# Kernel tuning notes

Measured on AMD Instinct MI355X. Metric: run time of the kernel, lower is better.

Reference implementation:

```python
import jax, jax.numpy as jnp
import numpy as np

B, P, C, O = 16, 19248, 81, 32
POS_THRESH, NEG_THRESH, NEGPOS_RATIO = 0.5, 0.4, 3
BBOX_ALPHA, CONF_ALPHA = 1.5, 1.0
VAR0, VAR1 = 0.1, 0.2  # SSD encoding variances


def setup_inputs() -> dict:
    key = jax.random.key(0)
    ks = jax.random.split(key, 7)
    loc_data = jax.random.normal(ks[0], (B, P, 4), dtype=jnp.float32)
    conf_data = jax.random.normal(ks[1], (B, P, C), dtype=jnp.float32)
    # priors in center form (cx, cy, w, h), all positive
    cxcy = jax.random.uniform(ks[2], (P, 2), minval=0.05, maxval=0.95)
    wh = jax.random.uniform(ks[3], (P, 2), minval=0.05, maxval=0.30)
    priors = jnp.concatenate([cxcy, wh], axis=-1).astype(jnp.float32)
    # gt boxes in point form (x1, y1, x2, y2), valid and inside [0,1]
    gcxcy = jax.random.uniform(ks[4], (B, O, 2), minval=0.1, maxval=0.9)
    gwh = jax.random.uniform(ks[5], (B, O, 2), minval=0.05, maxval=0.4)
    gt_boxes = jnp.clip(jnp.concatenate([gcxcy - gwh / 2, gcxcy + gwh / 2], axis=-1), 0.0, 1.0).astype(jnp.float32)
    gt_labels = jax.random.randint(ks[6], (B, O), 0, C - 1, dtype=jnp.int32)  # 0..79, bg is class 0 after +1
    return {"loc_data": loc_data, "conf_data": conf_data, "priors": priors,
            "gt_boxes": gt_boxes, "gt_labels": gt_labels}


def _point_form(boxes):
    # center form (cx,cy,w,h) -> point form (x1,y1,x2,y2)
    return jnp.concatenate([boxes[:, :2] - boxes[:, 2:] / 2,
                            boxes[:, :2] + boxes[:, 2:] / 2], axis=-1)


def _jaccard(a, b):
    # a: [O,4] point form, b: [P,4] point form -> IoU [O,P]
    lt = jnp.maximum(a[:, None, :2], b[None, :, :2])
    rb = jnp.minimum(a[:, None, 2:], b[None, :, 2:])
    inter = jnp.prod(jnp.clip(rb - lt, 0.0, None), axis=-1)
    area_a = jnp.prod(a[:, 2:] - a[:, :2], axis=-1)[:, None]
    area_b = jnp.prod(b[:, 2:] - b[:, :2], axis=-1)[None, :]
    return inter / (area_a + area_b - inter)


def _encode(matched, priors):
    # matched: [P,4] point form gt; priors: [P,4] center form
    g_cxcy = ((matched[:, :2] + matched[:, 2:]) / 2 - priors[:, :2]) / (VAR0 * priors[:, 2:])
    g_wh = jnp.log((matched[:, 2:] - matched[:, :2]) / priors[:, 2:]) / VAR1
    return jnp.concatenate([g_cxcy, g_wh], axis=-1)


def _match_one(truths, labels, priors):
    # truths: [O,4] point form, labels: [O] int, priors: [P,4] center form
    overlaps = _jaccard(truths, _point_form(priors))          # [O,P]
    best_truth_overlap = overlaps.max(axis=0)                  # [P]
    best_truth_idx = overlaps.argmax(axis=0)                   # [P]
    best_prior_idx = overlaps.argmax(axis=1)                   # [O]
    # ensure every gt is matched to its best prior
    best_truth_overlap = best_truth_overlap.at[best_prior_idx].set(2.0)
    best_truth_idx = best_truth_idx.at[best_prior_idx].set(jnp.arange(truths.shape[0]))
    matched = truths[best_truth_idx]                           # [P,4]
    conf = labels[best_truth_idx] + 1                          # [P]
    conf = jnp.where(best_truth_overlap < POS_THRESH, -1, conf)  # neutral
    conf = jnp.where(best_truth_overlap < NEG_THRESH, 0, conf)   # background
    loc = _encode(matched, priors)                             # [P,4]
    return loc, conf


def _multibox_loss(loc_data, conf_data, priors, gt_boxes, gt_labels):
    loc_t, conf_t = jax.vmap(_match_one, in_axes=(0, 0, None))(gt_boxes, gt_labels, priors)
    pos = conf_t > 0                                           # [B,P]
    # --- localization: smooth L1 on positives ---
    d = jnp.abs(loc_data - loc_t)
    sl1 = jnp.where(d < 1.0, 0.5 * d * d, d - 0.5)
    loss_B = jnp.sum(sl1 * pos[..., None].astype(sl1.dtype)) * BBOX_ALPHA
    # --- OHEM confidence loss ---
    logZ = jax.nn.logsumexp(conf_data, axis=-1)                # [B,P]
    loss_c = logZ - conf_data[..., 0]                          # log_sum_exp - background logit
    loss_c = jnp.where(pos | (conf_t < 0), 0.0, loss_c)
    order = jnp.argsort(-loss_c, axis=1)                       # descending
    idx_rank = jnp.argsort(order, axis=1)                      # rank of each prior
    num_pos = jnp.sum(pos, axis=1, keepdims=True)              # [B,1]
    num_neg = jnp.clip(NEGPOS_RATIO * num_pos, None, P - 1)
    neg = (idx_rank < num_neg) & (~pos) & (conf_t >= 0)
    ce = logZ - jnp.take_along_axis(conf_data, jnp.maximum(conf_t, 0)[..., None], axis=-1)[..., 0]
    loss_C = jnp.sum(ce * (pos | neg).astype(ce.dtype)) * CONF_ALPHA
    total_num_pos = jnp.sum(pos).astype(loc_data.dtype)
    return jnp.stack([loss_B, loss_C]) / total_num_pos


def reference(loc_data, conf_data, priors, gt_boxes, gt_labels):
    return _multibox_loss(loc_data, conf_data, priors, gt_boxes, gt_labels)
```

## Files before the change

kernel.cpp:

```cpp
#include <hip/hip_runtime.h>
#include <math.h>

#define B_ 16
#define P_ 19248
#define C_ 81
#define O_ 32
#define POS_TH 0.5f
#define NEG_TH 0.4f
#define RPB 128
#define TPB 1024
#define PQ  4812
#define BP_BLK (B_ * O_ * 4)
#define BT_BPB 76
#define OT 1024
#define NJ 19

__device__ __forceinline__ float sl1(float x) {
    float d = fabsf(x);
    return (d < 1.0f) ? 0.5f * d * d : d - 0.5f;
}

__device__ __forceinline__ float iou_gt_prior(float4 t, float4 pr) {
    float px1 = pr.x - pr.z * 0.5f;
    float py1 = pr.y - pr.w * 0.5f;
    float px2 = pr.x + pr.z * 0.5f;
    float py2 = pr.y + pr.w * 0.5f;
    float ltx = fmaxf(t.x, px1), lty = fmaxf(t.y, py1);
    float rbx = fminf(t.z, px2), rby = fminf(t.w, py2);
    float iw = fmaxf(rbx - ltx, 0.0f), ih = fmaxf(rby - lty, 0.0f);
    float inter = iw * ih;
    float area_t = (t.z - t.x) * (t.w - t.y);
    float area_p = (px2 - px1) * (py2 - py1);
    return inter / (area_t + area_p - inter);
}

template <int PER>
__device__ __forceinline__ void pick_top(const int* __restrict__ h, int kk, int tid,
                                         int* s_bin, int* s_kk, int* wsum) {
    const int lane = tid & 63, wid = tid >> 6;
    const int base = tid * PER;
    int v[PER]; int s = 0;
    #pragma unroll
    for (int j = 0; j < PER; ++j) { v[j] = h[base + j]; s += v[j]; }
    int x = s;
    #pragma unroll
    for (int d = 1; d < 64; d <<= 1) {
        int y = __shfl_down(x, d);
        if (lane + d < 64) x += y;
    }
    if (lane == 0) wsum[wid] = x;
    __syncthreads();
    int above = 0;
    #pragma unroll
    for (int w = 0; w < 16; ++w) if (w > wid) above += wsum[w];
    int T = (x - s) + above;
    if (T < kk && kk <= T + s) {
        int kl = kk - T, cum = 0;
        #pragma unroll
        for (int j = PER - 1; j >= 0; --j) {
            if (cum + v[j] >= kl) { *s_bin = base + j; *s_kk = kl - cum; break; }
            cum += v[j];
        }
    }
    __syncthreads();
}

template <int PER>
__device__ __forceinline__ void pick_bot(const int* __restrict__ h, int kk, int tid,
                                         int* s_bin, int* s_kk, int* wsum) {
    const int lane = tid & 63, wid = tid >> 6;
    const int base = tid * PER;
    int v[PER]; int s = 0;
    #pragma unroll
    for (int j = 0; j < PER; ++j) { v[j] = h[base + j]; s += v[j]; }
    int x = s;
    #pragma unroll
    for (int d = 1; d < 64; d <<= 1) {
        int y = __shfl_up(x, d);
        if (lane >= d) x += y;
    }
    if (lane == 63) wsum[wid] = x;
    __syncthreads();
    int below = 0;
    #pragma unroll
    for (int w = 0; w < 16; ++w) if (w < wid) below += wsum[w];
    int T = (x - s) + below;
    if (T < kk && kk <= T + s) {
        int kl = kk - T, cum = 0;
        #pragma unroll
        for (int j = 0; j < PER; ++j) {
            if (cum + v[j] >= kl) { *s_bin = base + j; *s_kk = kl - cum; break; }
            cum += v[j];
        }
    }
    __syncthreads();
}

__global__ void k_match(const float* __restrict__ priors,
                        const float* __restrict__ gt_boxes,
                        const int* __restrict__ gt_labels,
                        unsigned long long* __restrict__ best_key,
                        float* __restrict__ bt_ov,
                        int* __restrict__ bt_ix,
                        int* __restrict__ bt_lab) {
    const int bid = blockIdx.x;
    if (bid < BP_BLK) {
        int pair = bid >> 2, qtr = bid & 3;
        int b = pair >> 5, o = pair & 31;
        float4 t = ((const float4*)gt_boxes)[b * O_ + o];
        float bestv = -1.0f; int besti = 0;
        int pstart = qtr * PQ;
        for (int p = pstart + threadIdx.x; p < pstart + PQ; p += 256) {
            float4 pr = ((const float4*)priors)[p];
            float v = iou_gt_prior(t, pr);
            if (v > bestv) { bestv = v; besti = p; }
        }
        __shared__ float sv[256];
        __shared__ int   si[256];
        sv[threadIdx.x] = bestv; si[threadIdx.x] = besti;
        __syncthreads();
        for (int s = 128; s > 0; s >>= 1) {
            if (threadIdx.x < s) {
                float ov = sv[threadIdx.x + s]; int oi = si[threadIdx.x + s];
                if (ov > sv[threadIdx.x] ||
                    (ov == sv[threadIdx.x] && oi < si[threadIdx.x])) {
                    sv[threadIdx.x] = ov; si[threadIdx.x] = oi;
                }
            }
            __syncthreads();
        }
        if (threadIdx.x == 0) {
            unsigned long long key =
                ((unsigned long long)__float_as_uint(sv[0]) << 32) |
                (unsigned long long)(0xFFFFFFFFu - (unsigned int)si[0]);
            atomicMax(&best_key[pair], key);
        }
    } else {
        int idx = bid - BP_BLK;
        int b = idx / BT_BPB;
        int p = (idx % BT_BPB) * 256 + threadIdx.x;
        __shared__ float4 gt[O_];
        __shared__ int    gl[O_];
        if (threadIdx.x < O_) {
            gt[threadIdx.x] = ((const float4*)gt_boxes)[b * O_ + threadIdx.x];
            gl[threadIdx.x] = gt_labels[b * O_ + threadIdx.x];
        }
        __syncthreads();
        if (p >= P_) return;
        float4 pr = ((const float4*)priors)[p];
        float bestv = -1.0f; int besti = 0;
        for (int o = 0; o < O_; ++o) {
            float v = iou_gt_prior(gt[o], pr);
            if (v > bestv) { bestv = v; besti = o; }
        }
        size_t bp = (size_t)b * P_ + p;
        bt_ov[bp] = bestv;
        bt_ix[bp] = besti;
        bt_lab[bp] = gl[besti];
    }
}

__global__ __launch_bounds__(TPB, 8) void
k_main(const float* __restrict__ loc_data,
       const float* __restrict__ conf_data,
       const float* __restrict__ priors,
       const float* __restrict__ gt_boxes,
       const int* __restrict__ gt_labels,
       const unsigned long long* __restrict__ best_key,
       const float* __restrict__ bt_ov,
       const int* __restrict__ bt_ix,
       const int* __restrict__ bt_lab,
       float* __restrict__ lossc,
       float* __restrict__ ce_neg,
       int* __restrict__ num_pos,
       float* __restrict__ accum) {
    __shared__ float srow[RPB * C_];
    __shared__ int s_fp[2][O_];
    __shared__ int s_fl[2][O_];
    __shared__ float s_lB, s_ceP;
    __shared__ int s_np0, s_np1;
    const int row0 = blockIdx.x * RPB;
    const int b0 = row0 / P_;
    const int tid = threadIdx.x;
    const int w = tid >> 6;
    if (tid == 0) { s_lB = 0.0f; s_ceP = 0.0f; s_np0 = 0; s_np1 = 0; }

    {
        const float4* src = (const float4*)(conf_data + (size_t)row0 * C_);
        float4* dst4 = (float4*)srow;
        __builtin_amdgcn_global_load_lds(
            (const __attribute__((address_space(1))) void*)(src + tid),
            (__attribute__((address_space(3))) void*)(dst4 + (w << 6)),
            16, 0, 0);
        __builtin_amdgcn_global_load_lds(
            (const __attribute__((address_space(1))) void*)(src + 1024 + tid),
            (__attribute__((address_space(3))) void*)(dst4 + 1024 + (w << 6)),
            16, 0, 0);
        if (tid < 544) {
            __builtin_amdgcn_global_load_lds(
                (const __attribute__((address_space(1))) void*)(src + 2048 + tid),
                (__attribute__((address_space(3))) void*)(dst4 + 2048 + (w << 6)),
                16, 0, 0);
        }
    }
    if (tid < 2 * O_) {
        int half = tid >> 5, o = tid & 31;
        int bb = b0 + half;
        int fp = -1, fl = 0;
        if (bb < B_) {
            unsigned long long key = best_key[bb * O_ + o];
            fp = (int)(0xFFFFFFFFu - (unsigned int)(key & 0xFFFFFFFFu));
            fl = gt_labels[bb * O_ + o];
        }
        s_fp[half][o] = fp;
        s_fl[half][o] = fl;
    }
    __syncthreads();

    const int r = tid >> 3;
    const int q = tid & 7;
    const int bp = row0 + r;
    const int b = bp / P_;
    const int p = bp - b * P_;
    const float* row = srow + r * C_;
    const int j0 = 10 * q;

    float ma = row[j0], mb = row[j0 + 1];
    #pragma unroll
    for (int i = 2; i < 10; i += 2) {
        ma = fmaxf(ma, row[j0 + i]);
        mb = fmaxf(mb, row[j0 + i + 1]);
    }
    float m = fmaxf(ma, mb);
    if (q == 7) m = fmaxf(m, row[80]);
    m = fmaxf(m, __shfl_xor(m, 1));
    m = fmaxf(m, __shfl_xor(m, 2));
    m = fmaxf(m, __shfl_xor(m, 4));

    float sa = 0.f, sb = 0.f;
    #pragma unroll
    for (int i = 0; i < 10; i += 2) {
        sa += __expf(row[j0 + i] - m);
        sb += __expf(row[j0 + i + 1] - m);
    }
    float s = sa + sb;
    if (q == 7) s += __expf(row[80] - m);
    s += __shfl_xor(s, 1);
    s += __shfl_xor(s, 2);
    s += __shfl_xor(s, 4);
    float logZ = m + __logf(s);

    if (q == 0) {
        const int whichb = b - b0;
        int foo = -1;
        #pragma unroll
        for (int oo = O_ - 1; oo >= 0; --oo) {
            if (foo < 0 && s_fp[whichb][oo] == p) foo = oo;
        }
        int conf_t, ti = 0;
        bool pos;
        if (foo >= 0) {
            conf_t = s_fl[whichb][foo] + 1;
            pos = true;
            ti = foo;
        } else {
            float ov = bt_ov[bp];
            conf_t = bt_lab[bp] + 1;
            if (ov < POS_TH) conf_t = -1;
            if (ov < NEG_TH) conf_t = 0;
            pos = conf_t > 0;
            if (pos) ti = bt_ix[bp];
        }

        float lc = (pos || conf_t < 0) ? 0.0f : (logZ - row[0]);
        int cls = pos ? conf_t : 0;
        float ce = logZ - row[cls];

        lossc[bp] = lc;
        ce_neg[bp] = (conf_t == 0) ? ce : 0.0f;

        if (pos) {
            float4 t = ((const float4*)gt_boxes)[b * O_ + ti];
            float4 pr = ((const float4*)priors)[p];
            float mcx = (t.x + t.z) * 0.5f;
            float mcy = (t.y + t.w) * 0.5f;
            float gx = (mcx - pr.x) / (0.1f * pr.z);
            float gy = (mcy - pr.y) / (0.1f * pr.w);
            float gw = logf((t.z - t.x) / pr.z) / 0.2f;
            float gh = logf((t.w - t.y) / pr.w) / 0.2f;
            float4 ld = ((const float4*)loc_data)[bp];
            float sc2 = sl1(ld.x - gx) + sl1(ld.y - gy) + sl1(ld.z - gw) + sl1(ld.w - gh);
            atomicAdd(&s_lB, sc2);
            atomicAdd(&s_ceP, ce);
            if (b == b0) atomicAdd(&s_np0, 1); else atomicAdd(&s_np1, 1);
        }
    }
    __syncthreads();
    if (tid == 0) {
        if (s_lB != 0.0f) atomicAdd(&accum[0], s_lB);
        if (s_ceP != 0.0f) atomicAdd(&accum[1], s_ceP);
        if (s_np0) atomicAdd(&num_pos[b0], s_np0);
        if (s_np1) atomicAdd(&num_pos[b0 + 1], s_np1);
    }
}

__global__ __launch_bounds__(OT) void
k_ohem(const float* __restrict__ lossc, const float* __restrict__ ce_neg,
       const int* __restrict__ num_pos, const float* __restrict__ accum,
       float* __restrict__ ce_sum, int* __restrict__ done,
       float* __restrict__ out) {
    const int b = blockIdx.x;
    const int tid = threadIdx.x;
    const float* lc = lossc + (size_t)b * P_;
    const float* cn = ce_neg + (size_t)b * P_;
    __shared__ int h[2048];
    __shared__ int wsum[16];
    __shared__ int s_bin, s_kk;
    __shared__ float red[OT];

    int k = 3 * num_pos[b];
    if (k > P_ - 1) k = P_ - 1;

    float result = 0.0f;
    if (k > 0) {
        unsigned int fb[NJ]; float cv[NJ];
        #pragma unroll
        for (int j = 0; j < NJ; ++j) {
            int i = tid + j * OT;
            bool valid = (i < P_);
            fb[j] = valid ? __float_as_uint(lc[i]) : 0u;
            cv[j] = valid ? cn[i] : 0.0f;
        }
        h[tid] = 0; h[tid + 1024] = 0;
        __syncthreads();
        #pragma unroll
        for (int j = 0; j < NJ; ++j) atomicAdd(&h[fb[j] >> 21], 1);
        __syncthreads();
        pick_top<2>(h, k, tid, &s_bin, &s_kk, wsum);
        const unsigned int T = (unsigned int)s_bin;
        int kk = s_kk;

        h[tid] = 0; h[tid + 1024] = 0;
        __syncthreads();
        float sum = 0.0f;
        #pragma unroll
        for (int j = 0; j < NJ; ++j) {
            unsigned int bin = fb[j] >> 21;
            if (bin > T) sum += cv[j];
            else if (bin == T) atomicAdd(&h[(fb[j] >> 10) & 2047], 1);
        }
        __syncthreads();
        pick_top<2>(h, kk, tid, &s_bin, &s_kk, wsum);
        const unsigned int pre21 = (T << 11) | (unsigned int)s_bin;
        kk = s_kk;

        h[tid] = 0; h[tid + 1024] = 0;
        __syncthreads();
        #pragma unroll
        for (int j = 0; j < NJ; ++j)
            if ((fb[j] >> 10) == pre21) atomicAdd(&h[fb[j] & 1023], 1);
        __syncthreads();
        pick_top<2>(h, kk, tid, &s_bin, &s_kk, wsum);
        const unsigned int V = (pre21 << 10) | (unsigned int)s_bin;
        const int ee = h[s_bin];
        kk = s_kk;

        if (kk == ee) {
            #pragma unroll
            for (int j = 0; j < NJ; ++j)
                if ((fb[j] >> 21) == T && fb[j] >= V) sum += cv[j];
        } else {
            h[tid] = 0; h[tid + 1024] = 0;
            __syncthreads();
            #pragma unroll
            for (int j = 0; j < NJ; ++j)
                if (fb[j] == V) atomicAdd(&h[(tid + j * OT) >> 6], 1);
            __syncthreads();
            pick_bot<2>(h, kk, tid, &s_bin, &s_kk, wsum);
            const int d6 = s_bin;
            kk = s_kk;
            h[tid] = 0; h[tid + 1024] = 0;
            __syncthreads();
            #pragma unroll
            for (int j = 0; j < NJ; ++j) {
                int i = tid + j * OT;
                if (fb[j] == V && (i >> 6) == d6) atomicAdd(&h[i & 63], 1);
            }
            __syncthreads();
            pick_bot<2>(h, kk, tid, &s_bin, &s_kk, wsum);
            const int Istar = (d6 << 6) | s_bin;
            #pragma unroll
            for (int j = 0; j < NJ; ++j) {
                int i = tid + j * OT;
                if ((fb[j] >> 21) == T && (fb[j] > V || (fb[j] == V && i <= Istar)))
                    sum += cv[j];
            }
        }

        red[tid] = sum;
        __syncthreads();
        for (int s = OT / 2; s > 0; s >>= 1) {
            if (tid < s) red[tid] += red[tid + s];
            __syncthreads();
        }
        result = red[0];
    }

    if (tid == 0) {
        ce_sum[b] = result;
        __threadfence();
        int old = atomicAdd(done, 1);
        if (old == B_ - 1) {
            __threadfence();
            int tp = 0; float ns = 0.0f;
            for (int bb = 0; bb < B_; ++bb) { tp += num_pos[bb]; ns += ce_sum[bb]; }
            float inv = 1.0f / (float)tp;
            out[0] = accum[0] * 1.5f * inv;
            out[1] = (accum[1] + ns) * inv;
        }
    }
}

extern "C" void kernel_launch(void* const* d_in, const int* in_sizes, int n_in,
                              void* d_out, int out_size, void* d_ws, size_t ws_size,
                              hipStream_t stream) {
    const float* loc    = (const float*)d_in[0];
    const float* conf   = (const float*)d_in[1];
    const float* priors = (const float*)d_in[2];
    const float* gtb    = (const float*)d_in[3];
    const int*   gtl    = (const int*)d_in[4];
    float* out = (float*)d_out;

    const size_t BP = (size_t)B_ * P_;
    float* W = (float*)d_ws;
    float* bt_ov   = W;
    float* lossc   = W + BP;
    float* ce_neg  = W + 2 * BP;
    int*   bt_ix   = (int*)(W + 3 * BP);
    int*   bt_lab  = (int*)(W + 4 * BP);
    unsigned long long* best_key = (unsigned long long*)(W + 5 * BP);
    int*   num_pos = (int*)(best_key + B_ * O_);
    float* ce_sum  = (float*)(num_pos + B_);
    float* accum   = ce_sum + B_;
    int*   done    = (int*)(accum + 2);

    size_t zbytes = B_ * O_ * sizeof(unsigned long long) +
                    B_ * sizeof(int) + B_ * sizeof(float) +
                    2 * sizeof(float) + sizeof(int);
    hipMemsetAsync(best_key, 0, zbytes, stream);
    hipLaunchKernelGGL(k_match, dim3(BP_BLK + B_ * BT_BPB), dim3(256), 0, stream,
                       priors, gtb, gtl, best_key, bt_ov, bt_ix, bt_lab);
    hipLaunchKernelGGL(k_main, dim3((int)(BP / RPB)), dim3(TPB), 0, stream,
                       loc, conf, priors, gtb, gtl, best_key,
                       bt_ov, bt_ix, bt_lab, lossc, ce_neg, num_pos, accum);
    hipLaunchKernelGGL(k_ohem, dim3(B_), dim3(OT), 0, stream,
                       lossc, ce_neg, num_pos, accum, ce_sum, done, out);
}
```

Measured before the change: 119.4 us.

## Split k_main row tile into two halves to overlap LDS loads with compute

k_main now uses 512 threads and two 64-row LDS buffers. It issues the async global-to-LDS load for the second half while computing logsumexp and loss terms on the first half, so the conf_data load latency is hidden behind compute within a block. The trade-off is fewer threads per block, a lower occupancy hint in launch_bounds, and an extra barrier. Correctness relies on the second-half load having completed by the time the barrier after the first half is reached.

```diff
diff --git a/kernel.cpp b/kernel.cpp
--- a/kernel.cpp
+++ b/kernel.cpp
@@ -8,12 +8,15 @@
 #define POS_TH 0.5f
 #define NEG_TH 0.4f
 #define RPB 128
-#define TPB 1024
+#define TPB 512
 #define PQ  4812
 #define BP_BLK (B_ * O_ * 4)
 #define BT_BPB 76
 #define OT 1024
 #define NJ 19
+
+#define AS1 const __attribute__((address_space(1))) void*
+#define AS3 __attribute__((address_space(3))) void*
 
 __device__ __forceinline__ float sl1(float x) {
     float d = fabsf(x);
@@ -160,7 +163,97 @@
     }
 }
 
-__global__ __launch_bounds__(TPB, 8) void
+__device__ __forceinline__ void compute_half(
+    const float* __restrict__ buf, int rowbase, int b0,
+    const int s_fp[2][O_], const int s_fl[2][O_],
+    const float* __restrict__ loc_data, const float* __restrict__ priors,
+    const float* __restrict__ gt_boxes,
+    const float* __restrict__ bt_ov, const int* __restrict__ bt_ix,
+    const int* __restrict__ bt_lab,
+    float* __restrict__ lossc, float* __restrict__ ce_neg,
+    float* s_lB, float* s_ceP, int* s_np0, int* s_np1, int tid)
+{
+    const int r = tid >> 3;
+    const int q = tid & 7;
+    const int bp = rowbase + r;
+    const int b = bp / P_;
+    const int p = bp - b * P_;
+    const float* row = buf + r * C_;
+    const int j0 = 10 * q;
+
+    float ma = row[j0], mb = row[j0 + 1];
+    #pragma unroll
+    for (int i = 2; i < 10; i += 2) {
+        ma = fmaxf(ma, row[j0 + i]);
+        mb = fmaxf(mb, row[j0 + i + 1]);
+    }
+    float m = fmaxf(ma, mb);
+    if (q == 7) m = fmaxf(m, row[80]);
+    m = fmaxf(m, __shfl_xor(m, 1));
+    m = fmaxf(m, __shfl_xor(m, 2));
+    m = fmaxf(m, __shfl_xor(m, 4));
+
+    float sa = 0.f, sb = 0.f;
+    #pragma unroll
+    for (int i = 0; i < 10; i += 2) {
+        sa += __expf(row[j0 + i] - m);
+        sb += __expf(row[j0 + i + 1] - m);
+    }
+    float s = sa + sb;
+    if (q == 7) s += __expf(row[80] - m);
+    s += __shfl_xor(s, 1);
+    s += __shfl_xor(s, 2);
+    s += __shfl_xor(s, 4);
+    float logZ = m + __logf(s);
+
+    if (q == 0) {
+        const int whichb = b - b0;
+        int foo = -1;
+        #pragma unroll
+        for (int oo = O_ - 1; oo >= 0; --oo) {
+            if (foo < 0 && s_fp[whichb][oo] == p) foo = oo;
+        }
+        int conf_t, ti = 0;
+        bool pos;
+        if (foo >= 0) {
+            conf_t = s_fl[whichb][foo] + 1;
+            pos = true;
+            ti = foo;
+        } else {
+            float ov = bt_ov[bp];
+            conf_t = bt_lab[bp] + 1;
+            if (ov < POS_TH) conf_t = -1;
+            if (ov < NEG_TH) conf_t = 0;
+            pos = conf_t > 0;
+            if (pos) ti = bt_ix[bp];
+        }
+
+        float lc = (pos || conf_t < 0) ? 0.0f : (logZ - row[0]);
+        int cls = pos ? conf_t : 0;
+        float ce = logZ - row[cls];
+
+        lossc[bp] = lc;
+        ce_neg[bp] = (conf_t == 0) ? ce : 0.0f;
+
+        if (pos) {
+            float4 t = ((const float4*)gt_boxes)[b * O_ + ti];
+            float4 pr = ((const float4*)priors)[p];
+            float mcx = (t.x + t.z) * 0.5f;
+            float mcy = (t.y + t.w) * 0.5f;
+            float gx = (mcx - pr.x) / (0.1f * pr.z);
+            float gy = (mcy - pr.y) / (0.1f * pr.w);
+            float gw = logf((t.z - t.x) / pr.z) / 0.2f;
+            float gh = logf((t.w - t.y) / pr.w) / 0.2f;
+            float4 ld = ((const float4*)loc_data)[bp];
+            float sc2 = sl1(ld.x - gx) + sl1(ld.y - gy) + sl1(ld.z - gw) + sl1(ld.w - gh);
+            atomicAdd(s_lB, sc2);
+            atomicAdd(s_ceP, ce);
+            if (b == b0) atomicAdd(s_np0, 1); else atomicAdd(s_np1, 1);
+        }
+    }
+}
+
+__global__ __launch_bounds__(TPB, 6) void
 k_main(const float* __restrict__ loc_data,
        const float* __restrict__ conf_data,
        const float* __restrict__ priors,
@@ -174,7 +267,8 @@
        float* __restrict__ ce_neg,
        int* __restrict__ num_pos,
        float* __restrict__ accum) {
-    __shared__ float srow[RPB * C_];
+    __shared__ float srowA[64 * C_];
+    __shared__ float srowB[64 * C_];
     __shared__ int s_fp[2][O_];
     __shared__ int s_fl[2][O_];
     __shared__ float s_lB, s_ceP;
@@ -187,21 +281,14 @@
 
     {
         const float4* src = (const float4*)(conf_data + (size_t)row0 * C_);
-        float4* dst4 = (float4*)srow;
-        __builtin_amdgcn_global_load_lds(
-            (const __attribute__((address_space(1))) void*)(src + tid),
-            (__attribute__((address_space(3))) void*)(dst4 + (w << 6)),
-            16, 0, 0);
-        __builtin_amdgcn_global_load_lds(
-            (const __attribute__((address_space(1))) void*)(src + 1024 + tid),
-            (__attribute__((address_space(3))) void*)(dst4 + 1024 + (w << 6)),
-            16, 0, 0);
-        if (tid < 544) {
-            __builtin_amdgcn_global_load_lds(
-                (const __attribute__((address_space(1))) void*)(src + 2048 + tid),
-                (__attribute__((address_space(3))) void*)(dst4 + 2048 + (w << 6)),
-                16, 0, 0);
-        }
+        float4* dst4 = (float4*)srowA;
+        __builtin_amdgcn_global_load_lds((AS1)(src + tid),
+                                         (AS3)(dst4 + (w << 6)), 16, 0, 0);
+        __builtin_amdgcn_global_load_lds((AS1)(src + 512 + tid),
+                                         (AS3)(dst4 + 512 + (w << 6)), 16, 0, 0);
+        if (tid < 272)
+            __builtin_amdgcn_global_load_lds((AS1)(src + 1024 + tid),
+                                             (AS3)(dst4 + 1024 + (w << 6)), 16, 0, 0);
     }
     if (tid < 2 * O_) {
         int half = tid >> 5, o = tid & 31;
@@ -217,84 +304,25 @@
     }
     __syncthreads();
 
-    const int r = tid >> 3;
-    const int q = tid & 7;
-    const int bp = row0 + r;
-    const int b = bp / P_;
-    const int p = bp - b * P_;
-    const float* row = srow + r * C_;
-    const int j0 = 10 * q;
-
-    float ma = row[j0], mb = row[j0 + 1];
-    #pragma unroll
-    for (int i = 2; i < 10; i += 2) {
-        ma = fmaxf(ma, row[j0 + i]);
-        mb = fmaxf(mb, row[j0 + i + 1]);
-    }
-    float m = fmaxf(ma, mb);
-    if (q == 7) m = fmaxf(m, row[80]);
-    m = fmaxf(m, __shfl_xor(m, 1));
-    m = fmaxf(m, __shfl_xor(m, 2));
-    m = fmaxf(m, __shfl_xor(m, 4));
-
-    float sa = 0.f, sb = 0.f;
-    #pragma unroll
-    for (int i = 0; i < 10; i += 2) {
-        sa += __expf(row[j0 + i] - m);
-        sb += __expf(row[j0 + i + 1] - m);
-    }
-    float s = sa + sb;
-    if (q == 7) s += __expf(row[80] - m);
-    s += __shfl_xor(s, 1);
-    s += __shfl_xor(s, 2);
-    s += __shfl_xor(s, 4);
-    float logZ = m + __logf(s);
-
-    if (q == 0) {
-        const int whichb = b - b0;
-        int foo = -1;
-        #pragma unroll
-        for (int oo = O_ - 1; oo >= 0; --oo) {
-            if (foo < 0 && s_fp[whichb][oo] == p) foo = oo;
-        }
-        int conf_t, ti = 0;
-        bool pos;
-        if (foo >= 0) {
-            conf_t = s_fl[whichb][foo] + 1;
-            pos = true;
-            ti = foo;
-        } else {
-            float ov = bt_ov[bp];
-            conf_t = bt_lab[bp] + 1;
-            if (ov < POS_TH) conf_t = -1;
-            if (ov < NEG_TH) conf_t = 0;
-            pos = conf_t > 0;
-            if (pos) ti = bt_ix[bp];
-        }
-
-        float lc = (pos || conf_t < 0) ? 0.0f : (logZ - row[0]);
-        int cls = pos ? conf_t : 0;
-        float ce = logZ - row[cls];
-
-        lossc[bp] = lc;
-        ce_neg[bp] = (conf_t == 0) ? ce : 0.0f;
-
-        if (pos) {
-            float4 t = ((const float4*)gt_boxes)[b * O_ + ti];
-            float4 pr = ((const float4*)priors)[p];
-            float mcx = (t.x + t.z) * 0.5f;
-            float mcy = (t.y + t.w) * 0.5f;
-            float gx = (mcx - pr.x) / (0.1f * pr.z);
-            float gy = (mcy - pr.y) / (0.1f * pr.w);
-            float gw = logf((t.z - t.x) / pr.z) / 0.2f;
-            float gh = logf((t.w - t.y) / pr.w) / 0.2f;
-            float4 ld = ((const float4*)loc_data)[bp];
-            float sc2 = sl1(ld.x - gx) + sl1(ld.y - gy) + sl1(ld.z - gw) + sl1(ld.w - gh);
-            atomicAdd(&s_lB, sc2);
-            atomicAdd(&s_ceP, ce);
-            if (b == b0) atomicAdd(&s_np0, 1); else atomicAdd(&s_np1, 1);
-        }
-    }
+    {
+        const float4* src = (const float4*)(conf_data + (size_t)(row0 + 64) * C_);
+        float4* dst4 = (float4*)srowB;
+        __builtin_amdgcn_global_load_lds((AS1)(src + tid),
+                                         (AS3)(dst4 + (w << 6)), 16, 0, 0);
+        __builtin_amdgcn_global_load_lds((AS1)(src + 512 + tid),
+                                         (AS3)(dst4 + 512 + (w << 6)), 16, 0, 0);
+        if (tid < 272)
+            __builtin_amdgcn_global_load_lds((AS1)(src + 1024 + tid),
+                                             (AS3)(dst4 + 1024 + (w << 6)), 16, 0, 0);
+    }
+
+    compute_half(srowA, row0, b0, s_fp, s_fl, loc_data, priors, gt_boxes,
+                 bt_ov, bt_ix, bt_lab, lossc, ce_neg,
+                 &s_lB, &s_ceP, &s_np0, &s_np1, tid);
+    __syncthreads();
+    compute_half(srowB, row0 + 64, b0, s_fp, s_fl, loc_data, priors, gt_boxes,
+                 bt_ov, bt_ix, bt_lab, lossc, ce_neg,
+                 &s_lB, &s_ceP, &s_np0, &s_np1, tid);
     __syncthreads();
     if (tid == 0) {
         if (s_lB != 0.0f) atomicAdd(&accum[0], s_lB);
```

Measured after the change: 125.1 us. 4.8% more time.
